# Performance work log

Measured on AMD Instinct MI355X. Metric: run time of the kernel, lower is better.

The kernel has to match this reference:

```python
import jax, jax.numpy as jnp
import numpy as np

N_NODES = 50000
N_EDGES = 800000
NODE_FEAT = 3
EDGE_FEAT = 2
EMBED = 64
HIDDEN = 128
LAYERS = 4
POLY = 8


def setup_inputs() -> dict:
    key = jax.random.key(0)
    ks = jax.random.split(key, 24)
    s = 0.05
    inp = {
        "node_features": jax.random.normal(ks[0], (N_NODES, NODE_FEAT), jnp.float32),
        "edge_index": jax.random.randint(ks[1], (2, N_EDGES), 0, N_NODES, jnp.int32),
        "edge_features": jax.random.normal(ks[2], (N_EDGES, EDGE_FEAT), jnp.float32),
        "n": N_NODES,
        # node encoder MLP
        "enc_w1": jax.random.normal(ks[3], (NODE_FEAT, HIDDEN), jnp.float32) * s,
        "enc_b1": jnp.zeros((HIDDEN,), jnp.float32),
        "enc_w2": jax.random.normal(ks[4], (HIDDEN, EMBED), jnp.float32) * s,
        "enc_b2": jnp.zeros((EMBED,), jnp.float32),
        # per-layer conv message MLP (stacked over layers)
        "conv_w1": jax.random.normal(ks[5], (LAYERS, 2 * EMBED + EDGE_FEAT, EMBED), jnp.float32) * s,
        "conv_b1": jnp.zeros((LAYERS, EMBED), jnp.float32),
        "conv_w2": jax.random.normal(ks[6], (LAYERS, EMBED, EMBED), jnp.float32) * s,
        "conv_b2": jnp.zeros((LAYERS, EMBED), jnp.float32),
        # per-layer skip linear and layernorm
        "skip_w": jax.random.normal(ks[7], (LAYERS, EMBED, EMBED), jnp.float32) * s,
        "skip_b": jnp.zeros((LAYERS, EMBED), jnp.float32),
        "ln_g": jnp.ones((LAYERS, EMBED), jnp.float32),
        "ln_b": jnp.zeros((LAYERS, EMBED), jnp.float32),
        # polynomial head
        "head_w1": jax.random.normal(ks[8], (EMBED, EMBED), jnp.float32) * s,
        "head_b1": jnp.zeros((EMBED,), jnp.float32),
        "head_w2": jnp.zeros((EMBED, POLY), jnp.float32),  # zero-init per module
        "head_b2": jnp.ones((POLY,), jnp.float32),         # bias filled with 1.0
    }
    return inp


def _layernorm(x, g, b, eps=1e-5):
    mu = jnp.mean(x, axis=-1, keepdims=True)
    var = jnp.var(x, axis=-1, keepdims=True)
    return (x - mu) * jax.lax.rsqrt(var + eps) * g + b


def reference(node_features, edge_index, edge_features, n,
              enc_w1, enc_b1, enc_w2, enc_b2,
              conv_w1, conv_b1, conv_w2, conv_b2,
              skip_w, skip_b, ln_g, ln_b,
              head_w1, head_b1, head_w2, head_b2):
    rows, cols = edge_index[0], edge_index[1]
    # node encoder
    h = jax.nn.relu(node_features @ enc_w1 + enc_b1) @ enc_w2 + enc_b2  # [n, E]
    L = conv_w1.shape[0]
    for i in range(L):
        # gather + concat: [E_edges, 2*embed + edge_feat]
        msg_in = jnp.concatenate([h[rows], h[cols], edge_features], axis=-1)
        msg = jax.nn.relu(msg_in @ conv_w1[i] + conv_b1[i]) @ conv_w2[i] + conv_b2[i]
        agg = jax.ops.segment_sum(msg, rows, num_segments=n)  # scatter_add over source rows
        h_new = agg + h @ skip_w[i] + skip_b[i]
        h = jax.nn.relu(_layernorm(h_new, ln_g[i], ln_b[i]))
    # polynomial head
    return jax.nn.relu(h @ head_w1 + head_b1) @ head_w2 + head_b2  # [n, poly_degree]
```

## Files before the change

kernel.cpp:

```cpp
#include <hip/hip_runtime.h>

typedef unsigned short u16;
typedef __attribute__((ext_vector_type(8))) short bf16x8;
typedef __attribute__((ext_vector_type(4))) float f32x4;

#define MFMA16(a,b,c) __builtin_amdgcn_mfma_f32_16x16x32_bf16((a),(b),(c),0,0,0)

static __device__ __forceinline__ u16 f2bf(float x){
    unsigned int u = __float_as_uint(x);
    u += 0x7FFFu + ((u >> 16) & 1u);
    return (u16)(u >> 16);
}
static __device__ __forceinline__ float bf2f(short s){
    return __uint_as_float(((unsigned int)(u16)s) << 16);
}

static __device__ __forceinline__ bf16x8 load_bfrag(const float* __restrict__ W, int ldn, int n, int k0){
    bf16x8 r;
    #pragma unroll
    for (int j = 0; j < 8; ++j) r[j] = (short)f2bf(W[(k0 + j) * ldn + n]);
    return r;
}

__global__ __launch_bounds__(256) void enc_kernel(
    const float* __restrict__ X, const float* __restrict__ W1, const float* __restrict__ B1,
    const float* __restrict__ W2, const float* __restrict__ B2,
    const float* __restrict__ cW1, const float* __restrict__ cB1,
    u16* __restrict__ hbf, u16* __restrict__ Ubf, u16* __restrict__ Vbf, int N)
{
    __shared__ u16 sHid[64 * 136];
    __shared__ u16 sH[64 * 72];
    const int tid = threadIdx.x;
    const int w = tid >> 6, l = tid & 63, l15 = l & 15, quad = l >> 4;

    bf16x8 bW[4][4];
    #pragma unroll
    for (int ks = 0; ks < 4; ++ks)
        #pragma unroll
        for (int f = 0; f < 4; ++f)
            bW[ks][f] = load_bfrag(W2, 64, f * 16 + l15, ks * 32 + quad * 8);
    float b2v[4];
    #pragma unroll
    for (int f = 0; f < 4; ++f) b2v[f] = B2[f * 16 + l15];

    const int nbase = blockIdx.x * 64 + w * 16;

    {
        int e = l >> 2;
        int node = nbase + e; if (node > N - 1) node = N - 1;
        float x0 = X[node * 3], x1 = X[node * 3 + 1], x2 = X[node * 3 + 2];
        int k0 = (l & 3) * 32;
        u16* dst = sHid + (w * 16 + e) * 136 + k0;
        #pragma unroll
        for (int j = 0; j < 32; ++j){
            int k = k0 + j;
            float hv = x0 * W1[k] + x1 * W1[128 + k] + x2 * W1[256 + k] + B1[k];
            dst[j] = f2bf(hv > 0.f ? hv : 0.f);
        }
    }

    f32x4 acc[4];
    #pragma unroll
    for (int f = 0; f < 4; ++f){ acc[f][0]=b2v[f]; acc[f][1]=b2v[f]; acc[f][2]=b2v[f]; acc[f][3]=b2v[f]; }
    #pragma unroll
    for (int ks = 0; ks < 4; ++ks){
        bf16x8 a = *(const bf16x8*)&sHid[(w * 16 + l15) * 136 + ks * 32 + quad * 8];
        #pragma unroll
        for (int f = 0; f < 4; ++f) acc[f] = MFMA16(a, bW[ks][f], acc[f]);
    }
    #pragma unroll
    for (int r = 0; r < 4; ++r){
        int node = nbase + quad * 4 + r;
        #pragma unroll
        for (int f = 0; f < 4; ++f){
            u16 hb = f2bf(acc[f][r]);
            sH[(w * 16 + quad * 4 + r) * 72 + f * 16 + l15] = hb;
            if (node < N) hbf[(size_t)node * 64 + f * 16 + l15] = hb;
        }
    }

    bf16x8 bA[2][4], bB[2][4];
    #pragma unroll
    for (int kk = 0; kk < 2; ++kk)
        #pragma unroll
        for (int f = 0; f < 4; ++f){
            int n = f * 16 + l15, k0 = kk * 32 + quad * 8;
            bA[kk][f] = load_bfrag(cW1,           64, n, k0);
            bB[kk][f] = load_bfrag(cW1 + 64 * 64, 64, n, k0);
        }
    float b1n[4];
    #pragma unroll
    for (int f = 0; f < 4; ++f) b1n[f] = cB1[f * 16 + l15];

    bf16x8 a0 = *(const bf16x8*)&sH[(w * 16 + l15) * 72 + quad * 8];
    bf16x8 a1 = *(const bf16x8*)&sH[(w * 16 + l15) * 72 + 32 + quad * 8];

    f32x4 ua[4], va[4];
    #pragma unroll
    for (int f = 0; f < 4; ++f){
        ua[f][0]=b1n[f]; ua[f][1]=b1n[f]; ua[f][2]=b1n[f]; ua[f][3]=b1n[f];
        va[f][0]=0.f; va[f][1]=0.f; va[f][2]=0.f; va[f][3]=0.f;
    }
    #pragma unroll
    for (int f = 0; f < 4; ++f){ ua[f] = MFMA16(a0, bA[0][f], ua[f]); va[f] = MFMA16(a0, bB[0][f], va[f]); }
    #pragma unroll
    for (int f = 0; f < 4; ++f){ ua[f] = MFMA16(a1, bA[1][f], ua[f]); va[f] = MFMA16(a1, bB[1][f], va[f]); }

    #pragma unroll
    for (int r = 0; r < 4; ++r){
        int node = nbase + quad * 4 + r;
        if (node < N){
            #pragma unroll
            for (int f = 0; f < 4; ++f){
                Ubf[(size_t)node * 64 + f * 16 + l15] = f2bf(ua[f][r]);
                Vbf[(size_t)node * 64 + f * 16 + l15] = f2bf(va[f][r]);
            }
        }
    }
}

__global__ __launch_bounds__(256) void countB_kernel(const int* __restrict__ rows,
                                                     int* __restrict__ countsB, int E, int NB){
    __shared__ int c[1024];
    for (int i = threadIdx.x; i < NB; i += 256) c[i] = 0;
    __syncthreads();
    for (int i = blockIdx.x * 256 + threadIdx.x; i < E; i += gridDim.x * 256)
        atomicAdd(&c[rows[i] >> 6], 1);
    __syncthreads();
    for (int i = threadIdx.x; i < NB; i += 256){
        int v = c[i];
        if (v) atomicAdd(&countsB[i], v);
    }
}

__global__ __launch_bounds__(1024) void scanB_kernel(const int* __restrict__ countsB,
                                                     int* __restrict__ offsets,
                                                     int* __restrict__ cursorB, int NB){
    __shared__ int sc[1024];
    const int tid = threadIdx.x;
    int x = (tid < NB) ? countsB[tid] : 0;
    sc[tid] = x;
    __syncthreads();
    for (int d = 1; d < 1024; d <<= 1){
        int v = (tid >= d) ? sc[tid - d] : 0;
        __syncthreads();
        sc[tid] += v;
        __syncthreads();
    }
    int excl = sc[tid] - x;
    if (tid < NB){ offsets[tid] = excl; cursorB[tid] = excl; }
    if (tid == NB - 1) offsets[NB] = sc[tid];
}

#define CHUNK 8192

__global__ __launch_bounds__(1024) void binpack_kernel(
    const int* __restrict__ rows, const int* __restrict__ cols,
    const float* __restrict__ EF, int* __restrict__ cursorB,
    uint2* __restrict__ erec, int E)
{
    __shared__ u16 sRow[CHUNK];
    __shared__ u16 sPerm[CHUNK];
    __shared__ int cntA[1024], cntE[1024], cntC[1024], baseB[1024], sc[1024];
    const int tid = threadIdx.x;
    const int cbase = blockIdx.x * CHUNK;
    int C = E - cbase; if (C > CHUNK) C = CHUNK;
    if (C <= 0) return;

    cntA[tid] = 0;
    __syncthreads();
    for (int k = tid; k < C; k += 1024){
        int r = rows[cbase + k];
        sRow[k] = (u16)r;
        atomicAdd(&cntA[r >> 6], 1);
    }
    __syncthreads();
    sc[tid] = cntA[tid];
    __syncthreads();
    for (int d = 1; d < 1024; d <<= 1){
        int v = (tid >= d) ? sc[tid - d] : 0;
        __syncthreads();
        sc[tid] += v;
        __syncthreads();
    }
    int excl = sc[tid] - cntA[tid];
    cntE[tid] = excl;
    cntC[tid] = excl;
    if (cntA[tid] > 0) baseB[tid] = atomicAdd(&cursorB[tid], cntA[tid]);
    __syncthreads();
    for (int k = tid; k < C; k += 1024){
        int b = sRow[k] >> 6;
        int p = atomicAdd(&cntC[b], 1);
        sPerm[p] = (u16)k;
    }
    __syncthreads();
    for (int p = tid; p < C; p += 1024){
        int k = sPerm[p];
        int i = cbase + k;
        int r = sRow[k];
        int b = r >> 6;
        float2 ef = *(const float2*)&EF[2 * i];
        uint2 v;
        v.x = (unsigned)r | ((unsigned)cols[i] << 16);
        v.y = (unsigned)f2bf(ef.x) | ((unsigned)f2bf(ef.y) << 16);
        erec[baseB[b] + (p - cntE[b])] = v;
    }
}

#define ISSUE_UV(recv, U0, U1, V0, V1) do {                                  \
    int rr_ = (int)((recv).x & 0xFFFFu); if (rr_ == 0xFFFF) rr_ = 0;         \
    int cc_ = (int)((recv).x >> 16);                                         \
    const u16* pu_ = Ubf + (size_t)rr_ * 64 + quad * 8;                      \
    const u16* pv_ = Vbf + (size_t)cc_ * 64 + quad * 8;                      \
    U0 = *(const bf16x8*)(pu_);                                              \
    U1 = *(const bf16x8*)(pu_ + 32);                                         \
    V0 = *(const bf16x8*)(pv_);                                              \
    V1 = *(const bf16x8*)(pv_ + 32);                                         \
} while (0)

static __device__ __forceinline__ unsigned cvtpk(float a, float b){
    unsigned d;
    asm("v_cvt_pk_bf16_f32 %0, %1, %2" : "=v"(d) : "v"(a), "v"(b));
    return d;
}
#define PACK8(dst, x) do {                                                   \
    union { bf16x8 v; unsigned int d[4]; } _u;                               \
    _u.d[0] = cvtpk(x[0], x[1]); _u.d[1] = cvtpk(x[2], x[3]);                \
    _u.d[2] = cvtpk(x[4], x[5]); _u.d[3] = cvtpk(x[6], x[7]);                \
    dst = _u.v;                                                              \
} while (0)

__global__ __launch_bounds__(256, 3) void fused_kernel(
    const u16* __restrict__ Ubf, const u16* __restrict__ Vbf,
    const uint2* __restrict__ erec, const int* __restrict__ offsets,
    const float* __restrict__ W1,
    const float* __restrict__ W2, const float* __restrict__ B2,
    u16* __restrict__ hbf,
    const float* __restrict__ SW, const float* __restrict__ SB,
    const float* __restrict__ LG, const float* __restrict__ LB,
    const float* __restrict__ cW1, const float* __restrict__ cB1,
    u16* __restrict__ Un, u16* __restrict__ Vn,
    int N)
{
    __shared__ u16 sMsgT[2][64 * 72];
    __shared__ u16 sRowT[2][64];
    __shared__ u16 sH[64 * 72];
    const int tid = threadIdx.x;
    const int w = tid >> 6, l = tid & 63, l15 = l & 15, quad = l >> 4;
    const int w16 = w * 16;

    bf16x8 bW2[2][4];
    #pragma unroll
    for (int kk = 0; kk < 2; ++kk)
        #pragma unroll
        for (int f = 0; f < 4; ++f)
            bW2[kk][f] = load_bfrag(W2, 64, f * 16 + l15, kk * 32 + quad * 8);
    float bias2[4];
    #pragma unroll
    for (int f = 0; f < 4; ++f) bias2[f] = B2[f * 16 + l15];

    const float* Wc0 = W1 + 128 * 64;
    const float* Wc1 = W1 + 129 * 64;
    float e0l[8], e0h[8], e1l[8], e1h[8];
    #pragma unroll
    for (int j = 0; j < 8; ++j){
        int kl = quad * 8 + j;
        e0l[j] = Wc0[kl];       e0h[j] = Wc0[32 + kl];
        e1l[j] = Wc1[kl];       e1h[j] = Wc1[32 + kl];
    }

    const int b = blockIdx.x;
    const int start = offsets[b], end = offsets[b + 1];
    const int nt = (end - start + 63) >> 6;
    const int tgtrow = w16 + l15;

    f32x4 aggC[4] = {};

    auto LOADREC = [&](int t) -> uint2 {
        int e = start + t * 64 + w16 + l15;
        if (e < end) return erec[e];
        uint2 s; s.x = 0x0000FFFFu; s.y = 0u; return s;
    };

    if (nt > 0){
        uint2 recA = LOADREC(0);
        uint2 recB = (nt > 1) ? LOADREC(1) : recA;
        bf16x8 u0, u1, v0, v1;
        ISSUE_UV(recA, u0, u1, v0, v1);

        for (int t = 0; t < nt; ++t){
            uint2 recC = LOADREC(t + 2 < nt ? t + 2 : nt - 1);
            bf16x8 nu0, nu1, nv0, nv1;
            ISSUE_UV(recB, nu0, nu1, nv0, nv1);

            int rn_raw = (int)(recA.x & 0xFFFFu);
            float ef0 = bf2f((short)(recA.y & 0xFFFFu));
            float ef1 = bf2f((short)(recA.y >> 16));

            float xl[8], xh[8];
            #pragma unroll
            for (int j = 0; j < 8; ++j){
                float hA = fmaf(ef1, e1l[j], ef0 * e0l[j]);
                float hB = fmaf(ef1, e1h[j], ef0 * e0h[j]);
                xl[j] = fmaxf(hA + bf2f(u0[j]) + bf2f(v0[j]), 0.f);
                xh[j] = fmaxf(hB + bf2f(u1[j]) + bf2f(v1[j]), 0.f);
            }
            bf16x8 a0, a1;
            PACK8(a0, xl);
            PACK8(a1, xh);

            f32x4 m[4];
            #pragma unroll
            for (int f = 0; f < 4; ++f){ m[f][0]=bias2[f]; m[f][1]=bias2[f]; m[f][2]=bias2[f]; m[f][3]=bias2[f]; }
            #pragma unroll
            for (int f = 0; f < 4; ++f) m[f] = MFMA16(a0, bW2[0][f], m[f]);
            #pragma unroll
            for (int f = 0; f < 4; ++f) m[f] = MFMA16(a1, bW2[1][f], m[f]);

            const int buf = t & 1;
            #pragma unroll
            for (int f = 0; f < 4; ++f){
                uint2 wv;
                wv.x = cvtpk(m[f][0], m[f][1]);
                wv.y = cvtpk(m[f][2], m[f][3]);
                *(uint2*)&sMsgT[buf][(f * 16 + l15) * 72 + w16 + quad * 4] = wv;
            }
            if (quad == 0)
                sRowT[buf][w16 + l15] = (rn_raw == 0xFFFF) ? (u16)0xFFFF : (u16)(rn_raw & 63);

            __syncthreads();

            #pragma unroll
            for (int c = 0; c < 2; ++c){
                union { bf16x8 v; unsigned d[4]; } sfr;
                union { uint4 q; unsigned d[4]; } rv;
                rv.q = *(const uint4*)&sRowT[buf][c * 32 + quad * 8];
                #pragma unroll
                for (int k = 0; k < 4; ++k){
                    unsigned d = rv.d[k];
                    unsigned lo = d & 0xFFFFu, hi = d >> 16;
                    sfr.d[k] = (lo == (unsigned)tgtrow ? 0x3F80u : 0u)
                             | (hi == (unsigned)tgtrow ? 0x3F800000u : 0u);
                }
                #pragma unroll
                for (int f = 0; f < 4; ++f){
                    bf16x8 mb = *(const bf16x8*)&sMsgT[buf][(f * 16 + l15) * 72 + c * 32 + quad * 8];
                    aggC[f] = MFMA16(sfr.v, mb, aggC[f]);
                }
            }

            recA = recB; recB = recC;
            u0 = nu0; u1 = nu1; v0 = nv0; v1 = nv1;
        }
    }

    bf16x8 bW[2][4];
    #pragma unroll
    for (int kk = 0; kk < 2; ++kk)
        #pragma unroll
        for (int f = 0; f < 4; ++f)
            bW[kk][f] = load_bfrag(SW, 64, f * 16 + l15, kk * 32 + quad * 8);
    float sb[4], lg[4], lb[4];
    #pragma unroll
    for (int f = 0; f < 4; ++f){
        int n = f * 16 + l15;
        sb[f] = SB[n]; lg[f] = LG[n]; lb[f] = LB[n];
    }

    const int nbase = b * 64 + w16;
    int na = nbase + l15; if (na > N - 1) na = N - 1;
    const u16* pa = hbf + (size_t)na * 64 + quad * 8;
    bf16x8 h0 = *(const bf16x8*)pa;
    bf16x8 h1 = *(const bf16x8*)(pa + 32);

    f32x4 acc[4] = {};
    #pragma unroll
    for (int f = 0; f < 4; ++f) acc[f] = MFMA16(h0, bW[0][f], acc[f]);
    #pragma unroll
    for (int f = 0; f < 4; ++f) acc[f] = MFMA16(h1, bW[1][f], acc[f]);

    float vals[4][4];
    #pragma unroll
    for (int r = 0; r < 4; ++r)
        #pragma unroll
        for (int f = 0; f < 4; ++f)
            vals[f][r] = acc[f][r] + sb[f] + aggC[f][r];

    #pragma unroll
    for (int r = 0; r < 4; ++r){
        float s  = vals[0][r] + vals[1][r] + vals[2][r] + vals[3][r];
        float sq = vals[0][r]*vals[0][r] + vals[1][r]*vals[1][r]
                 + vals[2][r]*vals[2][r] + vals[3][r]*vals[3][r];
        #pragma unroll
        for (int msk = 1; msk < 16; msk <<= 1){
            s  += __shfl_xor(s,  msk);
            sq += __shfl_xor(sq, msk);
        }
        float mean = s * (1.f / 64.f);
        float var  = sq * (1.f / 64.f) - mean * mean;
        float rstd = rsqrtf(var + 1e-5f);
        int node = nbase + quad * 4 + r;
        #pragma unroll
        for (int f = 0; f < 4; ++f){
            float hv = (vals[f][r] - mean) * rstd * lg[f] + lb[f];
            hv = hv > 0.f ? hv : 0.f;
            u16 hb = f2bf(hv);
            sH[(w16 + quad * 4 + r) * 72 + f * 16 + l15] = hb;
            if (node < N) hbf[(size_t)node * 64 + f * 16 + l15] = hb;
        }
    }

    if (cW1){
        bf16x8 bA[2][4], bB[2][4];
        #pragma unroll
        for (int kk = 0; kk < 2; ++kk)
            #pragma unroll
            for (int f = 0; f < 4; ++f){
                int n = f * 16 + l15, k0 = kk * 32 + quad * 8;
                bA[kk][f] = load_bfrag(cW1,           64, n, k0);
                bB[kk][f] = load_bfrag(cW1 + 64 * 64, 64, n, k0);
            }
        float b1n[4];
        #pragma unroll
        for (int f = 0; f < 4; ++f) b1n[f] = cB1[f * 16 + l15];

        bf16x8 a0 = *(const bf16x8*)&sH[(w16 + l15) * 72 + quad * 8];
        bf16x8 a1 = *(const bf16x8*)&sH[(w16 + l15) * 72 + 32 + quad * 8];

        f32x4 ua[4], va[4];
        #pragma unroll
        for (int f = 0; f < 4; ++f){
            ua[f][0]=b1n[f]; ua[f][1]=b1n[f]; ua[f][2]=b1n[f]; ua[f][3]=b1n[f];
            va[f][0]=0.f; va[f][1]=0.f; va[f][2]=0.f; va[f][3]=0.f;
        }
        #pragma unroll
        for (int f = 0; f < 4; ++f){ ua[f] = MFMA16(a0, bA[0][f], ua[f]); va[f] = MFMA16(a0, bB[0][f], va[f]); }
        #pragma unroll
        for (int f = 0; f < 4; ++f){ ua[f] = MFMA16(a1, bA[1][f], ua[f]); va[f] = MFMA16(a1, bB[1][f], va[f]); }

        #pragma unroll
        for (int r = 0; r < 4; ++r){
            int node = nbase + quad * 4 + r;
            if (node < N){
                #pragma unroll
                for (int f = 0; f < 4; ++f){
                    Un[(size_t)node * 64 + f * 16 + l15] = f2bf(ua[f][r]);
                    Vn[(size_t)node * 64 + f * 16 + l15] = f2bf(va[f][r]);
                }
            }
        }
    }
}

__global__ __launch_bounds__(256) void head_kernel(
    const u16* __restrict__ hbf,
    const float* __restrict__ W1, const float* __restrict__ B1,
    const float* __restrict__ W2, const float* __restrict__ B2,
    float* __restrict__ out, int N)
{
    __shared__ u16 sT[64 * 72];
    const int tid = threadIdx.x;
    const int w = tid >> 6, l = tid & 63, l15 = l & 15, quad = l >> 4;

    bf16x8 bW1[2][4];
    #pragma unroll
    for (int kk = 0; kk < 2; ++kk)
        #pragma unroll
        for (int f = 0; f < 4; ++f)
            bW1[kk][f] = load_bfrag(W1, 64, f * 16 + l15, kk * 32 + quad * 8);
    float b1v[4];
    #pragma unroll
    for (int f = 0; f < 4; ++f) b1v[f] = B1[f * 16 + l15];

    bf16x8 bW2[2];
    #pragma unroll
    for (int kk = 0; kk < 2; ++kk)
        #pragma unroll
        for (int j = 0; j < 8; ++j){
            int k = kk * 32 + quad * 8 + j;
            bW2[kk][j] = (l15 < 8) ? (short)f2bf(W2[k * 8 + l15]) : (short)0;
        }
    float b2v = (l15 < 8) ? B2[l15] : 0.f;

    const int nbase = blockIdx.x * 64 + w * 16;
    int na = nbase + l15; if (na > N - 1) na = N - 1;
    const u16* pa = hbf + (size_t)na * 64 + quad * 8;
    bf16x8 a0 = *(const bf16x8*)pa;
    bf16x8 a1 = *(const bf16x8*)(pa + 32);

    f32x4 acc[4];
    #pragma unroll
    for (int f = 0; f < 4; ++f){ acc[f][0]=b1v[f]; acc[f][1]=b1v[f]; acc[f][2]=b1v[f]; acc[f][3]=b1v[f]; }
    #pragma unroll
    for (int f = 0; f < 4; ++f) acc[f] = MFMA16(a0, bW1[0][f], acc[f]);
    #pragma unroll
    for (int f = 0; f < 4; ++f) acc[f] = MFMA16(a1, bW1[1][f], acc[f]);

    u16* myT = sT + (w * 16) * 72;
    #pragma unroll
    for (int f = 0; f < 4; ++f)
        #pragma unroll
        for (int r = 0; r < 4; ++r){
            float v = acc[f][r] > 0.f ? acc[f][r] : 0.f;
            myT[(quad * 4 + r) * 72 + f * 16 + l15] = f2bf(v);
        }

    f32x4 o = { b2v, b2v, b2v, b2v };
    #pragma unroll
    for (int kk = 0; kk < 2; ++kk){
        bf16x8 a = *(const bf16x8*)&myT[l15 * 72 + kk * 32 + quad * 8];
        o = MFMA16(a, bW2[kk], o);
    }
    #pragma unroll
    for (int r = 0; r < 4; ++r){
        int node = nbase + quad * 4 + r;
        if (node < N && l15 < 8)
            out[(size_t)node * 8 + l15] = o[r];
    }
}

extern "C" void kernel_launch(void* const* d_in, const int* in_sizes, int n_in,
                              void* d_out, int out_size, void* d_ws, size_t ws_size,
                              hipStream_t stream)
{
    const float* X      = (const float*)d_in[0];
    const int*   EI     = (const int*)d_in[1];
    const float* EF     = (const float*)d_in[2];
    const float* encW1  = (const float*)d_in[4];
    const float* encB1  = (const float*)d_in[5];
    const float* encW2  = (const float*)d_in[6];
    const float* encB2  = (const float*)d_in[7];
    const float* convW1 = (const float*)d_in[8];
    const float* convB1 = (const float*)d_in[9];
    const float* convW2 = (const float*)d_in[10];
    const float* convB2 = (const float*)d_in[11];
    const float* skipW  = (const float*)d_in[12];
    const float* skipB  = (const float*)d_in[13];
    const float* lnG    = (const float*)d_in[14];
    const float* lnB    = (const float*)d_in[15];
    const float* headW1 = (const float*)d_in[16];
    const float* headB1 = (const float*)d_in[17];
    const float* headW2 = (const float*)d_in[18];
    const float* headB2 = (const float*)d_in[19];

    const int N = in_sizes[0] / 3;
    const int E = in_sizes[1] / 2;
    const int L = in_sizes[8] / (130 * 64);
    const int* rows = EI;
    const int* cols = EI + E;

    const int NB = (N + 63) / 64;

    auto align256 = [](size_t x){ return (x + 255) & ~(size_t)255; };
    char* p = (char*)d_ws;
    u16* hbf   = (u16*)p;           p += align256((size_t)N * 64 * 2);
    u16* Ubuf0 = (u16*)p;           p += align256((size_t)N * 64 * 2);
    u16* Vbuf0 = (u16*)p;           p += align256((size_t)N * 64 * 2);
    u16* Ubuf1 = (u16*)p;           p += align256((size_t)N * 64 * 2);
    u16* Vbuf1 = (u16*)p;           p += align256((size_t)N * 64 * 2);
    uint2* erec = (uint2*)p;        p += align256((size_t)E * 8);
    int* countsB = (int*)p;         p += align256(1024 * 4);
    int* offsets = (int*)p;         p += align256(1032 * 4);
    int* cursorB = (int*)p;         p += align256(1024 * 4);

    hipMemsetAsync(countsB, 0, (size_t)NB * sizeof(int), stream);
    countB_kernel<<<256, 256, 0, stream>>>(rows, countsB, E, NB);
    scanB_kernel<<<1, 1024, 0, stream>>>(countsB, offsets, cursorB, NB);
    binpack_kernel<<<(E + CHUNK - 1) / CHUNK, 1024, 0, stream>>>(rows, cols, EF, cursorB, erec, E);

    enc_kernel<<<NB, 256, 0, stream>>>(X, encW1, encB1, encW2, encB2,
                                       convW1, convB1, hbf, Ubuf0, Vbuf0, N);

    u16* Ucur = Ubuf0; u16* Vcur = Vbuf0;
    u16* Ualt = Ubuf1; u16* Valt = Vbuf1;
    for (int li = 0; li < L; ++li){
        const float* w1n = (li + 1 < L) ? convW1 + (size_t)(li + 1) * 130 * 64 : nullptr;
        const float* b1n = (li + 1 < L) ? convB1 + (li + 1) * 64 : nullptr;
        fused_kernel<<<NB, 256, 0, stream>>>(Ucur, Vcur, erec, offsets,
            convW1 + (size_t)li * 130 * 64,
            convW2 + (size_t)li * 64 * 64, convB2 + li * 64,
            hbf,
            skipW + (size_t)li * 64 * 64, skipB + li * 64,
            lnG + li * 64, lnB + li * 64,
            w1n, b1n, Ualt, Valt, N);
        u16* t;
        t = Ucur; Ucur = Ualt; Ualt = t;
        t = Vcur; Vcur = Valt; Valt = t;
    }
    head_kernel<<<NB, 256, 0, stream>>>(hbf, headW1, headB1, headW2, headB2,
                                        (float*)d_out, N);
}
```

Measured before the change: 327.1 us.

## Split edge tiles across two warp groups in fused GNN layer kernel

Doubles the fused layer kernel's block to 512 threads and splits each block's edge tiles between two 4-warp groups that alternate tiles, each with its own double-buffered shared-memory staging. The partial aggregations are combined through shared memory before one group runs the skip-linear and layernorm epilogue. The next-layer U/V projection is also split so each group computes one of the two outputs. The aim is more concurrent gather latency hiding and fewer serial tile iterations per block, at the cost of extra block-wide barriers, larger shared memory, and possibly lower occupancy under the new launch bounds.

```diff
diff --git a/kernel.cpp b/kernel.cpp
--- a/kernel.cpp
+++ b/kernel.cpp
@@ -230,7 +230,7 @@
     dst = _u.v;                                                              \
 } while (0)
 
-__global__ __launch_bounds__(256, 3) void fused_kernel(
+__global__ __launch_bounds__(512, 6) void fused_kernel(
     const u16* __restrict__ Ubf, const u16* __restrict__ Vbf,
     const uint2* __restrict__ erec, const int* __restrict__ offsets,
     const float* __restrict__ W1,
@@ -242,12 +242,15 @@
     u16* __restrict__ Un, u16* __restrict__ Vn,
     int N)
 {
-    __shared__ u16 sMsgT[2][64 * 72];
-    __shared__ u16 sRowT[2][64];
-    __shared__ u16 sH[64 * 72];
+    __shared__ u16 sMsg[4][64 * 72];
+    __shared__ u16 sRow[4][64];
+    float* comb = (float*)&sMsg[0][0];
+    u16*   sH   = &sMsg[0][8704];
+
     const int tid = threadIdx.x;
     const int w = tid >> 6, l = tid & 63, l15 = l & 15, quad = l >> 4;
-    const int w16 = w * 16;
+    const int wq = w & 3, grp = w >> 2;
+    const int wq16 = wq * 16;
 
     bf16x8 bW2[2][4];
     #pragma unroll
@@ -272,24 +275,25 @@
     const int b = blockIdx.x;
     const int start = offsets[b], end = offsets[b + 1];
     const int nt = (end - start + 63) >> 6;
-    const int tgtrow = w16 + l15;
+    const int nr = (nt + 1) >> 1;
+    const int tgtrow = wq16 + l15;
 
     f32x4 aggC[4] = {};
 
     auto LOADREC = [&](int t) -> uint2 {
-        int e = start + t * 64 + w16 + l15;
+        int e = start + t * 64 + wq16 + l15;
         if (e < end) return erec[e];
         uint2 s; s.x = 0x0000FFFFu; s.y = 0u; return s;
     };
 
-    if (nt > 0){
-        uint2 recA = LOADREC(0);
-        uint2 recB = (nt > 1) ? LOADREC(1) : recA;
+    if (nr > 0){
+        uint2 recA = LOADREC(grp);
+        uint2 recB = LOADREC(grp + 2);
         bf16x8 u0, u1, v0, v1;
         ISSUE_UV(recA, u0, u1, v0, v1);
 
-        for (int t = 0; t < nt; ++t){
-            uint2 recC = LOADREC(t + 2 < nt ? t + 2 : nt - 1);
+        for (int r = 0; r < nr; ++r){
+            uint2 recC = LOADREC(2 * r + grp + 4);
             bf16x8 nu0, nu1, nv0, nv1;
             ISSUE_UV(recB, nu0, nu1, nv0, nv1);
 
@@ -317,16 +321,16 @@
             #pragma unroll
             for (int f = 0; f < 4; ++f) m[f] = MFMA16(a1, bW2[1][f], m[f]);
 
-            const int buf = t & 1;
+            const int bi = grp * 2 + (r & 1);
             #pragma unroll
             for (int f = 0; f < 4; ++f){
                 uint2 wv;
                 wv.x = cvtpk(m[f][0], m[f][1]);
                 wv.y = cvtpk(m[f][2], m[f][3]);
-                *(uint2*)&sMsgT[buf][(f * 16 + l15) * 72 + w16 + quad * 4] = wv;
+                *(uint2*)&sMsg[bi][(f * 16 + l15) * 72 + wq16 + quad * 4] = wv;
             }
             if (quad == 0)
-                sRowT[buf][w16 + l15] = (rn_raw == 0xFFFF) ? (u16)0xFFFF : (u16)(rn_raw & 63);
+                sRow[bi][wq16 + l15] = (rn_raw == 0xFFFF) ? (u16)0xFFFF : (u16)(rn_raw & 63);
 
             __syncthreads();
 
@@ -334,7 +338,7 @@
             for (int c = 0; c < 2; ++c){
                 union { bf16x8 v; unsigned d[4]; } sfr;
                 union { uint4 q; unsigned d[4]; } rv;
-                rv.q = *(const uint4*)&sRowT[buf][c * 32 + quad * 8];
+                rv.q = *(const uint4*)&sRow[bi][c * 32 + quad * 8];
                 #pragma unroll
                 for (int k = 0; k < 4; ++k){
                     unsigned d = rv.d[k];
@@ -344,7 +348,7 @@
                 }
                 #pragma unroll
                 for (int f = 0; f < 4; ++f){
-                    bf16x8 mb = *(const bf16x8*)&sMsgT[buf][(f * 16 + l15) * 72 + c * 32 + quad * 8];
+                    bf16x8 mb = *(const bf16x8*)&sMsg[bi][(f * 16 + l15) * 72 + c * 32 + quad * 8];
                     aggC[f] = MFMA16(sfr.v, mb, aggC[f]);
                 }
             }
@@ -354,99 +358,113 @@
         }
     }
 
-    bf16x8 bW[2][4];
-    #pragma unroll
-    for (int kk = 0; kk < 2; ++kk)
+    __syncthreads();
+    if (grp == 1){
         #pragma unroll
         for (int f = 0; f < 4; ++f)
-            bW[kk][f] = load_bfrag(SW, 64, f * 16 + l15, kk * 32 + quad * 8);
-    float sb[4], lg[4], lb[4];
-    #pragma unroll
-    for (int f = 0; f < 4; ++f){
-        int n = f * 16 + l15;
-        sb[f] = SB[n]; lg[f] = LG[n]; lb[f] = LB[n];
-    }
-
-    const int nbase = b * 64 + w16;
-    int na = nbase + l15; if (na > N - 1) na = N - 1;
-    const u16* pa = hbf + (size_t)na * 64 + quad * 8;
-    bf16x8 h0 = *(const bf16x8*)pa;
-    bf16x8 h1 = *(const bf16x8*)(pa + 32);
-
-    f32x4 acc[4] = {};
-    #pragma unroll
-    for (int f = 0; f < 4; ++f) acc[f] = MFMA16(h0, bW[0][f], acc[f]);
-    #pragma unroll
-    for (int f = 0; f < 4; ++f) acc[f] = MFMA16(h1, bW[1][f], acc[f]);
-
-    float vals[4][4];
-    #pragma unroll
-    for (int r = 0; r < 4; ++r)
+            #pragma unroll
+            for (int r = 0; r < 4; ++r)
+                comb[(wq16 + quad * 4 + r) * 68 + f * 16 + l15] = aggC[f][r];
+    }
+    __syncthreads();
+
+    const int nbase = b * 64 + wq16;
+
+    if (grp == 0){
         #pragma unroll
         for (int f = 0; f < 4; ++f)
-            vals[f][r] = acc[f][r] + sb[f] + aggC[f][r];
-
-    #pragma unroll
-    for (int r = 0; r < 4; ++r){
-        float s  = vals[0][r] + vals[1][r] + vals[2][r] + vals[3][r];
-        float sq = vals[0][r]*vals[0][r] + vals[1][r]*vals[1][r]
-                 + vals[2][r]*vals[2][r] + vals[3][r]*vals[3][r];
-        #pragma unroll
-        for (int msk = 1; msk < 16; msk <<= 1){
-            s  += __shfl_xor(s,  msk);
-            sq += __shfl_xor(sq, msk);
-        }
-        float mean = s * (1.f / 64.f);
-        float var  = sq * (1.f / 64.f) - mean * mean;
-        float rstd = rsqrtf(var + 1e-5f);
-        int node = nbase + quad * 4 + r;
+            #pragma unroll
+            for (int r = 0; r < 4; ++r)
+                aggC[f][r] += comb[(wq16 + quad * 4 + r) * 68 + f * 16 + l15];
+
+        bf16x8 bW[2][4];
+        #pragma unroll
+        for (int kk = 0; kk < 2; ++kk)
+            #pragma unroll
+            for (int f = 0; f < 4; ++f)
+                bW[kk][f] = load_bfrag(SW, 64, f * 16 + l15, kk * 32 + quad * 8);
+        float sb[4], lg[4], lb[4];
         #pragma unroll
         for (int f = 0; f < 4; ++f){
-            float hv = (vals[f][r] - mean) * rstd * lg[f] + lb[f];
-            hv = hv > 0.f ? hv : 0.f;
-            u16 hb = f2bf(hv);
-            sH[(w16 + quad * 4 + r) * 72 + f * 16 + l15] = hb;
-            if (node < N) hbf[(size_t)node * 64 + f * 16 + l15] = hb;
-        }
-    }
+            int n = f * 16 + l15;
+            sb[f] = SB[n]; lg[f] = LG[n]; lb[f] = LB[n];
+        }
+
+        int na = nbase + l15; if (na > N - 1) na = N - 1;
+        const u16* pa = hbf + (size_t)na * 64 + quad * 8;
+        bf16x8 h0 = *(const bf16x8*)pa;
+        bf16x8 h1 = *(const bf16x8*)(pa + 32);
+
+        f32x4 acc[4] = {};
+        #pragma unroll
+        for (int f = 0; f < 4; ++f) acc[f] = MFMA16(h0, bW[0][f], acc[f]);
+        #pragma unroll
+        for (int f = 0; f < 4; ++f) acc[f] = MFMA16(h1, bW[1][f], acc[f]);
+
+        float vals[4][4];
+        #pragma unroll
+        for (int r = 0; r < 4; ++r)
+            #pragma unroll
+            for (int f = 0; f < 4; ++f)
+                vals[f][r] = acc[f][r] + sb[f] + aggC[f][r];
+
+        #pragma unroll
+        for (int r = 0; r < 4; ++r){
+            float s  = vals[0][r] + vals[1][r] + vals[2][r] + vals[3][r];
+            float sq = vals[0][r]*vals[0][r] + vals[1][r]*vals[1][r]
+                     + vals[2][r]*vals[2][r] + vals[3][r]*vals[3][r];
+            #pragma unroll
+            for (int msk = 1; msk < 16; msk <<= 1){
+                s  += __shfl_xor(s,  msk);
+                sq += __shfl_xor(sq, msk);
+            }
+            float mean = s * (1.f / 64.f);
+            float var  = sq * (1.f / 64.f) - mean * mean;
+            float rstd = rsqrtf(var + 1e-5f);
+            int node = nbase + quad * 4 + r;
+            #pragma unroll
+            for (int f = 0; f < 4; ++f){
+                float hv = (vals[f][r] - mean) * rstd * lg[f] + lb[f];
+                hv = hv > 0.f ? hv : 0.f;
+                u16 hb = f2bf(hv);
+                sH[(wq16 + quad * 4 + r) * 72 + f * 16 + l15] = hb;
+                if (node < N) hbf[(size_t)node * 64 + f * 16 + l15] = hb;
+            }
+        }
+    }
+    __syncthreads();
 
     if (cW1){
-        bf16x8 bA[2][4], bB[2][4];
+        const float* Wsel = (grp == 0) ? cW1 : (cW1 + 64 * 64);
+        bf16x8 bS[2][4];
         #pragma unroll
         for (int kk = 0; kk < 2; ++kk)
             #pragma unroll
-            for (int f = 0; f < 4; ++f){
-                int n = f * 16 + l15, k0 = kk * 32 + quad * 8;
-                bA[kk][f] = load_bfrag(cW1,           64, n, k0);
-                bB[kk][f] = load_bfrag(cW1 + 64 * 64, 64, n, k0);
-            }
+            for (int f = 0; f < 4; ++f)
+                bS[kk][f] = load_bfrag(Wsel, 64, f * 16 + l15, kk * 32 + quad * 8);
         float b1n[4];
         #pragma unroll
-        for (int f = 0; f < 4; ++f) b1n[f] = cB1[f * 16 + l15];
-
-        bf16x8 a0 = *(const bf16x8*)&sH[(w16 + l15) * 72 + quad * 8];
-        bf16x8 a1 = *(const bf16x8*)&sH[(w16 + l15) * 72 + 32 + quad * 8];
-
-        f32x4 ua[4], va[4];
-        #pragma unroll
-        for (int f = 0; f < 4; ++f){
-            ua[f][0]=b1n[f]; ua[f][1]=b1n[f]; ua[f][2]=b1n[f]; ua[f][3]=b1n[f];
-            va[f][0]=0.f; va[f][1]=0.f; va[f][2]=0.f; va[f][3]=0.f;
-        }
-        #pragma unroll
-        for (int f = 0; f < 4; ++f){ ua[f] = MFMA16(a0, bA[0][f], ua[f]); va[f] = MFMA16(a0, bB[0][f], va[f]); }
-        #pragma unroll
-        for (int f = 0; f < 4; ++f){ ua[f] = MFMA16(a1, bA[1][f], ua[f]); va[f] = MFMA16(a1, bB[1][f], va[f]); }
-
+        for (int f = 0; f < 4; ++f) b1n[f] = (grp == 0) ? cB1[f * 16 + l15] : 0.f;
+
+        bf16x8 a0 = *(const bf16x8*)&sH[(wq16 + l15) * 72 + quad * 8];
+        bf16x8 a1 = *(const bf16x8*)&sH[(wq16 + l15) * 72 + 32 + quad * 8];
+
+        f32x4 oa[4];
+        #pragma unroll
+        for (int f = 0; f < 4; ++f){ oa[f][0]=b1n[f]; oa[f][1]=b1n[f]; oa[f][2]=b1n[f]; oa[f][3]=b1n[f]; }
+        #pragma unroll
+        for (int f = 0; f < 4; ++f) oa[f] = MFMA16(a0, bS[0][f], oa[f]);
+        #pragma unroll
+        for (int f = 0; f < 4; ++f) oa[f] = MFMA16(a1, bS[1][f], oa[f]);
+
+        u16* dst = (grp == 0) ? Un : Vn;
         #pragma unroll
         for (int r = 0; r < 4; ++r){
             int node = nbase + quad * 4 + r;
             if (node < N){
                 #pragma unroll
-                for (int f = 0; f < 4; ++f){
-                    Un[(size_t)node * 64 + f * 16 + l15] = f2bf(ua[f][r]);
-                    Vn[(size_t)node * 64 + f * 16 + l15] = f2bf(va[f][r]);
-                }
+                for (int f = 0; f < 4; ++f)
+                    dst[(size_t)node * 64 + f * 16 + l15] = f2bf(oa[f][r]);
             }
         }
     }
@@ -576,7 +594,7 @@
     for (int li = 0; li < L; ++li){
         const float* w1n = (li + 1 < L) ? convW1 + (size_t)(li + 1) * 130 * 64 : nullptr;
         const float* b1n = (li + 1 < L) ? convB1 + (li + 1) * 64 : nullptr;
-        fused_kernel<<<NB, 256, 0, stream>>>(Ucur, Vcur, erec, offsets,
+        fused_kernel<<<NB, 512, 0, stream>>>(Ucur, Vcur, erec, offsets,
             convW1 + (size_t)li * 130 * 64,
             convW2 + (size_t)li * 64 * 64, convB2 + li * 64,
             hbf,
```

After: 1.232 ms. +276.6%, slower.

## Process edge tiles in pairs per barrier with quad-buffered shared memory

Applied to the files above, without the earlier changes.

The edge loop now handles two 64-edge tiles per iteration, so there is one __syncthreads per pair instead of one per tile. Message and row buffers become 4-way (double-buffered pairs), and sH is aliased into the message buffer to save LDS. The edge-feature weights are held as packed bf16 rather than fp32 to free registers, and launch bounds rise to 4 blocks per CU. The aim is fewer barriers, deeper gather prefetch, and higher occupancy, at the cost of more live registers and bf16 rounding of those edge weights.

```diff
diff --git a/kernel.cpp b/kernel.cpp
--- a/kernel.cpp
+++ b/kernel.cpp
@@ -230,7 +230,60 @@
     dst = _u.v;                                                              \
 } while (0)
 
-__global__ __launch_bounds__(256, 3) void fused_kernel(
+#define COMPUTE_MSG(rec, U0, U1, V0, V1, msgbuf, rowbuf) do {                \
+    int rn_raw_ = (int)((rec).x & 0xFFFFu);                                  \
+    float ef0_ = bf2f((short)((rec).y & 0xFFFFu));                           \
+    float ef1_ = bf2f((short)((rec).y >> 16));                               \
+    float xl_[8], xh_[8];                                                    \
+    _Pragma("unroll")                                                        \
+    for (int j = 0; j < 8; ++j){                                             \
+        float hA_ = fmaf(ef1_, bf2f(e1lo[j]), ef0_ * bf2f(e0lo[j]));         \
+        float hB_ = fmaf(ef1_, bf2f(e1hi[j]), ef0_ * bf2f(e0hi[j]));         \
+        xl_[j] = fmaxf(hA_ + bf2f((U0)[j]) + bf2f((V0)[j]), 0.f);            \
+        xh_[j] = fmaxf(hB_ + bf2f((U1)[j]) + bf2f((V1)[j]), 0.f);            \
+    }                                                                        \
+    bf16x8 a0_, a1_;                                                         \
+    PACK8(a0_, xl_); PACK8(a1_, xh_);                                        \
+    f32x4 m_[4];                                                             \
+    _Pragma("unroll")                                                        \
+    for (int f = 0; f < 4; ++f){ m_[f][0]=bias2[f]; m_[f][1]=bias2[f]; m_[f][2]=bias2[f]; m_[f][3]=bias2[f]; } \
+    _Pragma("unroll")                                                        \
+    for (int f = 0; f < 4; ++f) m_[f] = MFMA16(a0_, bW2[0][f], m_[f]);       \
+    _Pragma("unroll")                                                        \
+    for (int f = 0; f < 4; ++f) m_[f] = MFMA16(a1_, bW2[1][f], m_[f]);       \
+    _Pragma("unroll")                                                        \
+    for (int f = 0; f < 4; ++f){                                             \
+        uint2 wv_;                                                           \
+        wv_.x = cvtpk(m_[f][0], m_[f][1]);                                   \
+        wv_.y = cvtpk(m_[f][2], m_[f][3]);                                   \
+        *(uint2*)&(msgbuf)[(f * 16 + l15) * 72 + w16 + quad * 4] = wv_;      \
+    }                                                                        \
+    if (quad == 0)                                                           \
+        (rowbuf)[w16 + l15] = (rn_raw_ == 0xFFFF) ? (u16)0xFFFF : (u16)(rn_raw_ & 63); \
+} while (0)
+
+#define SCATTER(msgbuf, rowbuf) do {                                         \
+    _Pragma("unroll")                                                        \
+    for (int c = 0; c < 2; ++c){                                             \
+        union { bf16x8 v; unsigned d[4]; } sfr_;                             \
+        union { uint4 q; unsigned d[4]; } rv_;                               \
+        rv_.q = *(const uint4*)&(rowbuf)[c * 32 + quad * 8];                 \
+        _Pragma("unroll")                                                    \
+        for (int k = 0; k < 4; ++k){                                         \
+            unsigned d_ = rv_.d[k];                                          \
+            unsigned lo_ = d_ & 0xFFFFu, hi_ = d_ >> 16;                     \
+            sfr_.d[k] = (lo_ == (unsigned)tgtrow ? 0x3F80u : 0u)             \
+                      | (hi_ == (unsigned)tgtrow ? 0x3F800000u : 0u);        \
+        }                                                                    \
+        _Pragma("unroll")                                                    \
+        for (int f = 0; f < 4; ++f){                                         \
+            bf16x8 mb_ = *(const bf16x8*)&(msgbuf)[(f * 16 + l15) * 72 + c * 32 + quad * 8]; \
+            aggC[f] = MFMA16(sfr_.v, mb_, aggC[f]);                          \
+        }                                                                    \
+    }                                                                        \
+} while (0)
+
+__global__ __launch_bounds__(256, 4) void fused_kernel(
     const u16* __restrict__ Ubf, const u16* __restrict__ Vbf,
     const uint2* __restrict__ erec, const int* __restrict__ offsets,
     const float* __restrict__ W1,
@@ -242,9 +295,10 @@
     u16* __restrict__ Un, u16* __restrict__ Vn,
     int N)
 {
-    __shared__ u16 sMsgT[2][64 * 72];
-    __shared__ u16 sRowT[2][64];
-    __shared__ u16 sH[64 * 72];
+    __shared__ u16 sMsg[4][64 * 72];
+    __shared__ u16 sRow[4][64];
+    u16* sH = &sMsg[0][0];
+
     const int tid = threadIdx.x;
     const int w = tid >> 6, l = tid & 63, l15 = l & 15, quad = l >> 4;
     const int w16 = w * 16;
@@ -261,17 +315,18 @@
 
     const float* Wc0 = W1 + 128 * 64;
     const float* Wc1 = W1 + 129 * 64;
-    float e0l[8], e0h[8], e1l[8], e1h[8];
+    bf16x8 e0lo, e0hi, e1lo, e1hi;
     #pragma unroll
     for (int j = 0; j < 8; ++j){
         int kl = quad * 8 + j;
-        e0l[j] = Wc0[kl];       e0h[j] = Wc0[32 + kl];
-        e1l[j] = Wc1[kl];       e1h[j] = Wc1[32 + kl];
+        e0lo[j] = (short)f2bf(Wc0[kl]);      e0hi[j] = (short)f2bf(Wc0[32 + kl]);
+        e1lo[j] = (short)f2bf(Wc1[kl]);      e1hi[j] = (short)f2bf(Wc1[32 + kl]);
     }
 
     const int b = blockIdx.x;
     const int start = offsets[b], end = offsets[b + 1];
     const int nt = (end - start + 63) >> 6;
+    const int nr = (nt + 1) >> 1;
     const int tgtrow = w16 + l15;
 
     f32x4 aggC[4] = {};
@@ -282,77 +337,37 @@
         uint2 s; s.x = 0x0000FFFFu; s.y = 0u; return s;
     };
 
-    if (nt > 0){
-        uint2 recA = LOADREC(0);
-        uint2 recB = (nt > 1) ? LOADREC(1) : recA;
-        bf16x8 u0, u1, v0, v1;
-        ISSUE_UV(recA, u0, u1, v0, v1);
-
-        for (int t = 0; t < nt; ++t){
-            uint2 recC = LOADREC(t + 2 < nt ? t + 2 : nt - 1);
-            bf16x8 nu0, nu1, nv0, nv1;
-            ISSUE_UV(recB, nu0, nu1, nv0, nv1);
-
-            int rn_raw = (int)(recA.x & 0xFFFFu);
-            float ef0 = bf2f((short)(recA.y & 0xFFFFu));
-            float ef1 = bf2f((short)(recA.y >> 16));
-
-            float xl[8], xh[8];
+    if (nr > 0){
+        uint2 rA0 = LOADREC(0), rB0 = LOADREC(1);
+        uint2 rA1 = LOADREC(2), rB1 = LOADREC(3);
+        bf16x8 uA[4], uB[4];
+        ISSUE_UV(rA0, uA[0], uA[1], uA[2], uA[3]);
+        ISSUE_UV(rB0, uB[0], uB[1], uB[2], uB[3]);
+
+        for (int r = 0; r < nr; ++r){
+            uint2 rA2 = LOADREC(2 * r + 4), rB2 = LOADREC(2 * r + 5);
+            const int pi = (r & 1) * 2;
+
+            bf16x8 nA[4];
+            ISSUE_UV(rA1, nA[0], nA[1], nA[2], nA[3]);
+            COMPUTE_MSG(rA0, uA[0], uA[1], uA[2], uA[3], sMsg[pi], sRow[pi]);
+
+            bf16x8 nB[4];
+            ISSUE_UV(rB1, nB[0], nB[1], nB[2], nB[3]);
+            COMPUTE_MSG(rB0, uB[0], uB[1], uB[2], uB[3], sMsg[pi + 1], sRow[pi + 1]);
+
+            __syncthreads();
+
+            SCATTER(sMsg[pi], sRow[pi]);
+            SCATTER(sMsg[pi + 1], sRow[pi + 1]);
+
+            rA0 = rA1; rB0 = rB1; rA1 = rA2; rB1 = rB2;
             #pragma unroll
-            for (int j = 0; j < 8; ++j){
-                float hA = fmaf(ef1, e1l[j], ef0 * e0l[j]);
-                float hB = fmaf(ef1, e1h[j], ef0 * e0h[j]);
-                xl[j] = fmaxf(hA + bf2f(u0[j]) + bf2f(v0[j]), 0.f);
-                xh[j] = fmaxf(hB + bf2f(u1[j]) + bf2f(v1[j]), 0.f);
-            }
-            bf16x8 a0, a1;
-            PACK8(a0, xl);
-            PACK8(a1, xh);
-
-            f32x4 m[4];
-            #pragma unroll
-            for (int f = 0; f < 4; ++f){ m[f][0]=bias2[f]; m[f][1]=bias2[f]; m[f][2]=bias2[f]; m[f][3]=bias2[f]; }
-            #pragma unroll
-            for (int f = 0; f < 4; ++f) m[f] = MFMA16(a0, bW2[0][f], m[f]);
-            #pragma unroll
-            for (int f = 0; f < 4; ++f) m[f] = MFMA16(a1, bW2[1][f], m[f]);
-
-            const int buf = t & 1;
-            #pragma unroll
-            for (int f = 0; f < 4; ++f){
-                uint2 wv;
-                wv.x = cvtpk(m[f][0], m[f][1]);
-                wv.y = cvtpk(m[f][2], m[f][3]);
-                *(uint2*)&sMsgT[buf][(f * 16 + l15) * 72 + w16 + quad * 4] = wv;
-            }
-            if (quad == 0)
-                sRowT[buf][w16 + l15] = (rn_raw == 0xFFFF) ? (u16)0xFFFF : (u16)(rn_raw & 63);
-
-            __syncthreads();
-
-            #pragma unroll
-            for (int c = 0; c < 2; ++c){
-                union { bf16x8 v; unsigned d[4]; } sfr;
-                union { uint4 q; unsigned d[4]; } rv;
-                rv.q = *(const uint4*)&sRowT[buf][c * 32 + quad * 8];
-                #pragma unroll
-                for (int k = 0; k < 4; ++k){
-                    unsigned d = rv.d[k];
-                    unsigned lo = d & 0xFFFFu, hi = d >> 16;
-                    sfr.d[k] = (lo == (unsigned)tgtrow ? 0x3F80u : 0u)
-                             | (hi == (unsigned)tgtrow ? 0x3F800000u : 0u);
-                }
-                #pragma unroll
-                for (int f = 0; f < 4; ++f){
-                    bf16x8 mb = *(const bf16x8*)&sMsgT[buf][(f * 16 + l15) * 72 + c * 32 + quad * 8];
-                    aggC[f] = MFMA16(sfr.v, mb, aggC[f]);
-                }
-            }
-
-            recA = recB; recB = recC;
-            u0 = nu0; u1 = nu1; v0 = nv0; v1 = nv1;
-        }
-    }
+            for (int i = 0; i < 4; ++i){ uA[i] = nA[i]; uB[i] = nB[i]; }
+        }
+    }
+
+    __syncthreads();
 
     bf16x8 bW[2][4];
     #pragma unroll
```

After: 716.3 us. 119% more time.
